# Kernel tuning notes

Hardware: AMD Instinct MI355X
Metric: run time of the kernel (lower is better)

## Reference

```python
import jax, jax.numpy as jnp
import numpy as np

L = 2      # decoder layers
B = 4      # batch
T = 1000   # seq_len (mask built for this length)
C = 768    # input_dim / d_model
H = 12     # num_heads
DK = C // H
WIN = 100


def layernorm(x, g, b):
    m = x.mean(-1, keepdims=True)
    v = x.var(-1, keepdims=True)
    return (x - m) / jnp.sqrt(v + 1e-5) * g + b


def pos_encoding(t, c):
    # Transformer-XL / espnet RelPositionalEncoding table: relative positions t-1 .. -(t-1)
    rel = jnp.arange(t - 1, -t, -1, dtype=jnp.float32)          # (2t-1,)
    div = jnp.exp(-jnp.arange(0, c, 2, dtype=jnp.float32) * (np.log(10000.0) / c))
    ang = rel[:, None] * div[None, :]                            # (2t-1, c/2)
    pe = jnp.zeros((2 * t - 1, c), dtype=jnp.float32)
    pe = pe.at[:, 0::2].set(jnp.sin(ang)).at[:, 1::2].set(jnp.cos(ang))
    return pe


def rel_shift(x):
    # x: (B, H, T, 2T-1) -> (B, H, T, T), Transformer-XL relative shift
    b, h, t, p = x.shape
    xp = jnp.pad(x, ((0, 0), (0, 0), (0, 0), (1, 0)))
    xp = xp.reshape(b, h, p + 1, t)[:, :, 1:, :].reshape(b, h, t, p)
    return xp[..., :t]


def setup_inputs() -> dict:
    key = jax.random.key(0)
    ks = jax.random.split(key, 16)
    s = 0.02
    inp = {
        "x": jax.random.normal(ks[0], (B, T, C), dtype=jnp.float32),
        "Wq": jax.random.normal(ks[1], (L, C, C), dtype=jnp.float32) * s,
        "bq": jnp.zeros((L, C), dtype=jnp.float32),
        "Wk": jax.random.normal(ks[2], (L, C, C), dtype=jnp.float32) * s,
        "bk": jnp.zeros((L, C), dtype=jnp.float32),
        "Wv": jax.random.normal(ks[3], (L, C, C), dtype=jnp.float32) * s,
        "bv": jnp.zeros((L, C), dtype=jnp.float32),
        "Wo": jax.random.normal(ks[4], (L, C, C), dtype=jnp.float32) * s,
        "bo": jnp.zeros((L, C), dtype=jnp.float32),
        "Wp": jax.random.normal(ks[5], (L, C, C), dtype=jnp.float32) * s,   # linear_pos, no bias
        "pos_u": jax.random.normal(ks[6], (L, H, DK), dtype=jnp.float32) * s,
        "pos_v": jax.random.normal(ks[7], (L, H, DK), dtype=jnp.float32) * s,
        "ln1_g": jnp.ones((L, C), dtype=jnp.float32),
        "ln1_b": jnp.zeros((L, C), dtype=jnp.float32),
        "ln2_g": jnp.ones((L, C), dtype=jnp.float32),
        "ln2_b": jnp.zeros((L, C), dtype=jnp.float32),
        "W1": jax.random.normal(ks[8], (L, C, C), dtype=jnp.float32) * s,   # mlp_ratio = 1
        "b1": jnp.zeros((L, C), dtype=jnp.float32),
        "W2": jax.random.normal(ks[9], (L, C, C), dtype=jnp.float32) * s,
        "b2": jnp.zeros((L, C), dtype=jnp.float32),
    }
    # diagonal (banded) mask: True = blocked outside the attention window
    i = np.arange(T)
    blocked = np.abs(i[:, None] - i[None, :]) > (WIN // 2)
    inp["att_mask"] = jnp.asarray(blocked)
    return inp


def reference(x, att_mask, Wq, bq, Wk, bk, Wv, bv, Wo, bo, Wp, pos_u, pos_v,
              ln1_g, ln1_b, ln2_g, ln2_b, W1, b1, W2, b2):
    Bb, t, c = x.shape
    pe = pos_encoding(t, c)                       # (2T-1, C)
    h = x * jnp.sqrt(jnp.float32(c))              # xscale in RelPositionalEncoding
    for l in range(L):
        y = layernorm(h, ln1_g[l], ln1_b[l])
        q = (y @ Wq[l] + bq[l]).reshape(Bb, t, H, DK)
        k = (y @ Wk[l] + bk[l]).reshape(Bb, t, H, DK)
        v = (y @ Wv[l] + bv[l]).reshape(Bb, t, H, DK)
        p = (pe @ Wp[l]).reshape(2 * t - 1, H, DK)
        ac = jnp.einsum('bthd,bshd->bhts', q + pos_u[l], k)
        bd = rel_shift(jnp.einsum('bthd,phd->bhtp', q + pos_v[l], p))
        scores = (ac + bd) / jnp.sqrt(jnp.float32(DK))
        scores = jnp.where(att_mask[None, None], jnp.float32(-1e9), scores)
        attn = jax.nn.softmax(scores, axis=-1)
        o = jnp.einsum('bhts,bshd->bthd', attn, v).reshape(Bb, t, c)
        h = h + (o @ Wo[l] + bo[l])
        y2 = layernorm(h, ln2_g[l], ln2_b[l])
        h = h + (jax.nn.gelu(y2 @ W1[l] + b1[l]) @ W2[l] + b2[l])
    return h
```

## Files before the change

kernel.cpp:

```cpp
#include <hip/hip_runtime.h>
#include <math.h>

#define LNUM 2
#define BBATCH 4
#define TSEQ 1000
#define CDIM 768
#define HHEADS 12
#define DKK 64
#define PPOS (2*TSEQ-1)
#define HALFW 50
#define MROWS (BBATCH*TSEQ)
#define MPAD 4096
#define QKVDIM (3*CDIM)
#define NS 176

typedef __attribute__((ext_vector_type(8))) short s16x8;
typedef __attribute__((ext_vector_type(4))) short s16x4;
typedef __attribute__((ext_vector_type(4))) float f32x4;

#define LDSOFF(p) ((unsigned)(uintptr_t)(__attribute__((address_space(3))) const void*)(p))

__device__ __forceinline__ ushort f2bf(float x) {
    unsigned u = __float_as_uint(x);
    unsigned r = u + 0x7FFFu + ((u >> 16) & 1u);
    return (ushort)(r >> 16);
}
__device__ __forceinline__ float bf2f(ushort h) {
    return __uint_as_float(((unsigned)h) << 16);
}
__device__ __forceinline__ float gelu_f(float x) {
    float u = 0.7978845608028654f * (x + 0.044715f * x * x * x);
    return 0.5f * x * (1.f + tanhf(u));
}
__device__ __forceinline__ void gload_lds16(const void* g, void* l) {
    __builtin_amdgcn_global_load_lds(
        (const __attribute__((address_space(1))) void*)g,
        (__attribute__((address_space(3))) void*)l, 16, 0, 0);
}
__device__ __forceinline__ s16x4 tr_read(unsigned addr) {
    s16x4 d;
    asm volatile("ds_read_b64_tr_b16 %0, %1" : "=v"(d) : "v"(addr));
    return d;
}
__device__ __forceinline__ s16x4 tr_read128(unsigned addr) {
    s16x4 d;
    asm volatile("ds_read_b64_tr_b16 %0, %1 offset:128" : "=v"(d) : "v"(addr));
    return d;
}

__global__ __launch_bounds__(256) void transpose_pack(
    const float* __restrict__ Wq, const float* __restrict__ Wk,
    const float* __restrict__ Wv, const float* __restrict__ Wp,
    const float* __restrict__ Wo, const float* __restrict__ W1,
    const float* __restrict__ W2,
    ushort* __restrict__ Wtqkv, ushort* __restrict__ Wtp,
    ushort* __restrict__ Wto, ushort* __restrict__ Wt1, ushort* __restrict__ Wt2) {
    const int l = blockIdx.z / 7, m = blockIdx.z % 7;
    const float* srcs[7] = {Wq, Wk, Wv, Wp, Wo, W1, W2};
    const float* src = srcs[m] + (size_t)l * CDIM * CDIM;
    ushort* dst;
    if (m < 3)       dst = Wtqkv + (size_t)l * QKVDIM * CDIM + (size_t)m * CDIM * CDIM;
    else if (m == 3) dst = Wtp + (size_t)l * CDIM * CDIM;
    else if (m == 4) dst = Wto + (size_t)l * CDIM * CDIM;
    else if (m == 5) dst = Wt1 + (size_t)l * CDIM * CDIM;
    else             dst = Wt2 + (size_t)l * CDIM * CDIM;
    __shared__ float tile[32][33];
    const int tx = threadIdx.x, ty = threadIdx.y;
    const int c0 = blockIdx.x * 32, r0 = blockIdx.y * 32;
#pragma unroll
    for (int i = 0; i < 4; ++i)
        tile[ty + i * 8][tx] = src[(size_t)(r0 + ty + i * 8) * CDIM + c0 + tx];
    __syncthreads();
#pragma unroll
    for (int i = 0; i < 4; ++i)
        dst[(size_t)(c0 + ty + i * 8) * CDIM + r0 + tx] = f2bf(tile[tx][ty + i * 8]);
}

__global__ __launch_bounds__(256) void prep_small(ushort* __restrict__ pe,
                                                  const float* __restrict__ bq,
                                                  const float* __restrict__ bk,
                                                  const float* __restrict__ bv,
                                                  float* __restrict__ bqkv) {
    int idx = blockIdx.x * 256 + threadIdx.x;
    const int npair = 256 * (CDIM / 2);
    if (idx < npair) {
        int jloc = idx / (CDIM / 2);
        int m = idx - jloc * (CDIM / 2);
        int j = 896 + jloc;
        float rel = (float)(TSEQ - 1 - j);
        float div = expf(-(float)(2 * m) * (9.210340371976184f / (float)CDIM));
        float a = rel * div;
        pe[(size_t)j * CDIM + 2 * m]     = f2bf(sinf(a));
        pe[(size_t)j * CDIM + 2 * m + 1] = f2bf(cosf(a));
    }
    if (idx < LNUM * QKVDIM) {
        int l = idx / QKVDIM, c = idx - l * QKVDIM;
        float v;
        if (c < CDIM)            v = bq[l * CDIM + c];
        else if (c < 2 * CDIM)   v = bk[l * CDIM + c - CDIM];
        else                     v = bv[l * CDIM + c - 2 * CDIM];
        bqkv[idx] = v;
    }
}

__global__ __launch_bounds__(192) void ln_kernel(const float* __restrict__ in,
                                                 const float* __restrict__ g,
                                                 const float* __restrict__ bta,
                                                 ushort* __restrict__ y, float xscale) {
    const int row = blockIdx.x, tid = threadIdx.x;
    float4 v = *(const float4*)&in[(size_t)row * CDIM + tid * 4];
    v.x *= xscale; v.y *= xscale; v.z *= xscale; v.w *= xscale;
    float s  = v.x + v.y + v.z + v.w;
    float ss = v.x * v.x + v.y * v.y + v.z * v.z + v.w * v.w;
#pragma unroll
    for (int off = 32; off; off >>= 1) {
        s  += __shfl_xor(s, off);
        ss += __shfl_xor(ss, off);
    }
    __shared__ float sm[3], sq[3];
    const int wid = tid >> 6, lane = tid & 63;
    if (lane == 0) { sm[wid] = s; sq[wid] = ss; }
    __syncthreads();
    const float st  = sm[0] + sm[1] + sm[2];
    const float sst = sq[0] + sq[1] + sq[2];
    const float mean = st * (1.f / CDIM);
    const float var  = sst * (1.f / CDIM) - mean * mean;
    const float rstd = rsqrtf(var + 1e-5f);
    const float4 g4 = *(const float4*)&g[tid * 4];
    const float4 b4 = *(const float4*)&bta[tid * 4];
    ushort o0 = f2bf((v.x - mean) * rstd * g4.x + b4.x);
    ushort o1 = f2bf((v.y - mean) * rstd * g4.y + b4.y);
    ushort o2 = f2bf((v.z - mean) * rstd * g4.z + b4.z);
    ushort o3 = f2bf((v.w - mean) * rstd * g4.w + b4.w);
    uint2 pk; pk.x = (unsigned)o0 | ((unsigned)o1 << 16);
    pk.y = (unsigned)o2 | ((unsigned)o3 << 16);
    *(uint2*)&y[(size_t)row * CDIM + tid * 4] = pk;
}

template <int EPI>
__global__ __launch_bounds__(256, 3) void gemm64(const ushort* __restrict__ A,
                                                 const ushort* __restrict__ Bt,
                                                 const float* __restrict__ bias,
                                                 void* Out, int M, int ldo,
                                                 const float* resid, float rscale,
                                                 size_t zsB, size_t zsO) {
    __shared__ ushort lds[24576];
    const int tid = threadIdx.x;
    const int w = tid >> 6, lane = tid & 63;
    const int row0 = blockIdx.x * 64, col0 = blockIdx.y * 128;
    const size_t zb = blockIdx.z;
    Bt += zb * zsB;
    if (EPI == 2) Out = (void*)((float*)Out + zb * zsO);
    else          Out = (void*)((ushort*)Out + zb * zsO);

    const int srow8  = lane >> 3;
    const int schunk = (lane & 7) ^ srow8;

#define STAGE64(buf, k0)                                                        \
    {                                                                           \
        _Pragma("unroll")                                                       \
        for (int g = 0; g < 6; ++g) {                                           \
            const int grp = w * 6 + g;                                          \
            const int r = grp * 8 + srow8;                                      \
            const ushort* src = (grp < 8)                                       \
                ? A  + (size_t)(row0 + r) * CDIM + (k0) + schunk * 8            \
                : Bt + (size_t)(col0 + (r - 64)) * CDIM + (k0) + schunk * 8;    \
            gload_lds16(src, (char*)lds + (buf) * 24576 + grp * 1024);          \
        }                                                                       \
    }

    const int wm = (w >> 1) * 32, wn = (w & 1) * 64;
    const int lr = lane & 15, q = lane >> 4;
    f32x4 acc[2][4] = {};

    STAGE64(0, 0);
    __syncthreads();
    int cur = 0;
    for (int k0 = 0; k0 < CDIM; k0 += 64) {
        if (k0 + 64 < CDIM) STAGE64(cur ^ 1, k0 + 64);
        const int base = cur * 12288;
#pragma unroll
        for (int kk = 0; kk < 2; ++kk) {
            s16x8 af[2], bfr[4];
#pragma unroll
            for (int i = 0; i < 2; ++i) {
                const int r = wm + i * 16 + lr;
                af[i] = *(const s16x8*)&lds[base + r * 64 + ((((kk << 2) | q) ^ (r & 7)) << 3)];
            }
#pragma unroll
            for (int j = 0; j < 4; ++j) {
                const int r = 64 + wn + j * 16 + lr;
                bfr[j] = *(const s16x8*)&lds[base + r * 64 + ((((kk << 2) | q) ^ (r & 7)) << 3)];
            }
#pragma unroll
            for (int i = 0; i < 2; ++i)
#pragma unroll
                for (int j = 0; j < 4; ++j)
                    acc[i][j] = __builtin_amdgcn_mfma_f32_16x16x32_bf16(af[i], bfr[j], acc[i][j], 0, 0, 0);
        }
        __syncthreads();
        cur ^= 1;
    }
#undef STAGE64

    const int lrr = (lane >> 4) * 4;
    const int lc = lane & 15;
#pragma unroll
    for (int j = 0; j < 4; ++j) {
        const int col = col0 + wn + j * 16 + lc;
        const float bv = bias ? bias[col] : 0.f;
#pragma unroll
        for (int i = 0; i < 2; ++i) {
#pragma unroll
            for (int r = 0; r < 4; ++r) {
                const int row = row0 + wm + i * 16 + lrr + r;
                if (row >= M) continue;
                const float v = acc[i][j][r] + bv;
                if (EPI == 0)
                    ((ushort*)Out)[(size_t)row * ldo + col] = f2bf(v);
                else if (EPI == 1)
                    ((ushort*)Out)[(size_t)row * ldo + col] = f2bf(gelu_f(v));
                else {
                    float* p = (float*)Out + (size_t)row * ldo + col;
                    *p = resid[(size_t)row * ldo + col] * rscale + v;
                }
            }
        }
    }
}

template <int EPI>
__global__ __launch_bounds__(256, 3) void gemm128(const ushort* __restrict__ A,
                                                  const ushort* __restrict__ Bt,
                                                  const float* __restrict__ bias,
                                                  void* Out, int M, int ldo) {
    __shared__ ushort lds[16384];
    const int tid = threadIdx.x;
    const int w = tid >> 6, lane = tid & 63;
    const int row0 = blockIdx.x * 128, col0 = blockIdx.y * 128;
    const int srow   = lane >> 2;
    const int schunk = (lane & 3) ^ ((lane >> 3) & 3);
    const int wm = (w >> 1) * 64, wn = (w & 1) * 64;
    const int lr = lane & 15, q = lane >> 4;

#define STAGE128(buf, k0)                                                       \
    {                                                                           \
        _Pragma("unroll")                                                       \
        for (int g = 0; g < 4; ++g) {                                           \
            const int sp = w * 4 + g;                                           \
            const int r = sp * 16 + srow;                                       \
            const ushort* src = (r < 128)                                       \
                ? A  + (size_t)(row0 + r) * CDIM + (k0) + schunk * 8            \
                : Bt + (size_t)(col0 + (r - 128)) * CDIM + (k0) + schunk * 8;   \
            gload_lds16(src, (char*)lds + (buf) * 16384 + sp * 1024);           \
        }                                                                       \
    }

    f32x4 acc[4][4] = {};
    STAGE128(0, 0);
    __syncthreads();
    int cur = 0;
    for (int k0 = 0; k0 < CDIM; k0 += 32) {
        if (k0 + 32 < CDIM) STAGE128(cur ^ 1, k0 + 32);
        const int base = cur * 8192;
        s16x8 af[4], bfr[4];
#pragma unroll
        for (int i = 0; i < 4; ++i) {
            const int r = wm + i * 16 + lr;
            af[i] = *(const s16x8*)&lds[base + r * 32 + ((q ^ ((r >> 1) & 3)) << 3)];
        }
#pragma unroll
        for (int j = 0; j < 4; ++j) {
            const int r = 128 + wn + j * 16 + lr;
            bfr[j] = *(const s16x8*)&lds[base + r * 32 + ((q ^ ((r >> 1) & 3)) << 3)];
        }
#pragma unroll
        for (int i = 0; i < 4; ++i)
#pragma unroll
            for (int j = 0; j < 4; ++j)
                acc[i][j] = __builtin_amdgcn_mfma_f32_16x16x32_bf16(af[i], bfr[j], acc[i][j], 0, 0, 0);
        __syncthreads();
        cur ^= 1;
    }
#undef STAGE128

    const int crow0 = row0 + (w >> 1) * 64;
    const int ccol0 = col0 + (w & 1) * 64;
    const int lrr = (lane >> 4) * 4;
    const int lc = lane & 15;
#pragma unroll
    for (int j = 0; j < 4; ++j) {
        const int col = ccol0 + j * 16 + lc;
        const float bv = bias ? bias[col] : 0.f;
#pragma unroll
        for (int i = 0; i < 4; ++i) {
#pragma unroll
            for (int r = 0; r < 4; ++r) {
                const int row = crow0 + i * 16 + lrr + r;
                if (row >= M) continue;
                const float v = acc[i][j][r] + bv;
                if (EPI == 0)
                    ((ushort*)Out)[(size_t)row * ldo + col] = f2bf(v);
                else if (EPI == 1)
                    ((ushort*)Out)[(size_t)row * ldo + col] = f2bf(gelu_f(v));
            }
        }
    }
}

__global__ __launch_bounds__(256, 3) void attn_mfma(
    const ushort* __restrict__ qkv, const ushort* __restrict__ pb,
    const float* __restrict__ pos_u, const float* __restrict__ pos_v,
    ushort* __restrict__ o) {
    __shared__ __align__(16) char smem[51200];
    ushort* Kl   = (ushort*)smem;
    ushort* Pl   = (ushort*)smem;
    ushort* Vsub = (ushort*)(smem + 25600);
    ushort* Bd   = (ushort*)(smem + 37888);

    const int tid = threadIdx.x;
    const int w = tid >> 6, lane = tid & 63;
    const int t0 = blockIdx.x * 64;
    const int h = blockIdx.y, b = blockIdx.z;
    const int m0 = w * 16;
    const int lr = lane & 15, lk = (lane >> 4) * 8, q = lane >> 4;

    auto vsrc = [&](int sp) -> const ushort* {
        const int ob = sp * 1024 + lane * 16;
        const int d0c = ob / 6144;
        const int rem = ob - d0c * 6144;
        const int j = rem >> 5;
        const int halfo = (rem & 31) >> 4;
        int t = t0 - HALFW + j; t = t < 0 ? 0 : (t < TSEQ ? t : TSEQ - 1);
        return qkv + (size_t)(b * TSEQ + t) * QKVDIM + 2 * CDIM + h * DKK
               + (d0c & 1) * 16 + halfo * 8;
    };

    int tq = t0 + m0 + lr; tq = tq < TSEQ ? tq : TSEQ - 1;
    const ushort* qp = qkv + (size_t)(b * TSEQ + tq) * QKVDIM + h * DKK;
    s16x8 qr0 = *(const s16x8*)(qp + lk);
    s16x8 qr1 = *(const s16x8*)(qp + 32 + lk);
    const float* puB = pos_u + h * DKK;
    const float* pvB = pos_v + h * DKK;
    float puA[16], pvA[16];
    *(float4*)&puA[0]  = *(const float4*)(puB + lk);
    *(float4*)&puA[4]  = *(const float4*)(puB + lk + 4);
    *(float4*)&puA[8]  = *(const float4*)(puB + 32 + lk);
    *(float4*)&puA[12] = *(const float4*)(puB + 32 + lk + 4);
    *(float4*)&pvA[0]  = *(const float4*)(pvB + lk);
    *(float4*)&pvA[4]  = *(const float4*)(pvB + lk + 4);
    *(float4*)&pvA[8]  = *(const float4*)(pvB + 32 + lk);
    *(float4*)&pvA[12] = *(const float4*)(pvB + 32 + lk + 4);

    const ushort* pbh = pb + (size_t)949 * CDIM + h * DKK;
    s16x8 pfr[7][2];
#pragma unroll
    for (int uf = 0; uf < 7; ++uf) {
        pfr[uf][0] = *(const s16x8*)&pbh[(size_t)(uf * 16 + lr) * CDIM + lk];
        pfr[uf][1] = *(const s16x8*)&pbh[(size_t)(uf * 16 + lr) * CDIM + 32 + lk];
    }

#pragma unroll
    for (int g = 0; g < 3; ++g) {
        const int sp = w * 3 + g;
        gload_lds16(vsrc(sp), (char*)Vsub + sp * 1024);
    }

    {
        const int srow8 = lane >> 3;
        const int schunk = (lane & 7) ^ srow8;
#pragma unroll
        for (int g = 0; g < 6; ++g) {
            const int sp = w * 6 + g;
            if (sp < 22) {
                const int r = sp * 8 + srow8;
                int kb = t0 - HALFW + r; kb = kb < 0 ? 0 : (kb < TSEQ ? kb : TSEQ - 1);
                const ushort* src = qkv + (size_t)(b * TSEQ + kb) * QKVDIM + CDIM
                                    + h * DKK + schunk * 8;
                gload_lds16(src, (char*)Kl + sp * 1024);
            }
        }
    }

    s16x8 qu0, qu1, qv0, qv1;
#pragma unroll
    for (int e = 0; e < 8; ++e) {
        const float q0 = bf2f((ushort)qr0[e]), q1 = bf2f((ushort)qr1[e]);
        qu0[e] = (short)f2bf(q0 + puA[e]);
        qu1[e] = (short)f2bf(q1 + puA[8 + e]);
        qv0[e] = (short)f2bf(q0 + pvA[e]);
        qv1[e] = (short)f2bf(q1 + pvA[8 + e]);
    }
    __syncthreads();

    const f32x4 zero = {0.f, 0.f, 0.f, 0.f};
    f32x4 acS[11], acB[7];
    __builtin_amdgcn_s_setprio(1);
#pragma unroll
    for (int uf = 0; uf < 7; ++uf) {
        acB[uf] = __builtin_amdgcn_mfma_f32_16x16x32_bf16(qv0, pfr[uf][0], zero, 0, 0, 0);
        acB[uf] = __builtin_amdgcn_mfma_f32_16x16x32_bf16(qv1, pfr[uf][1], acB[uf], 0, 0, 0);
    }
#pragma unroll
    for (int jf = 0; jf < 11; ++jf) {
        const int rr = jf * 16 + lr;
        const int sw = rr & 7;
        s16x8 k0 = *(const s16x8*)&Kl[rr * 64 + (((q)     ^ sw) << 3)];
        s16x8 k1 = *(const s16x8*)&Kl[rr * 64 + (((q | 4) ^ sw) << 3)];
        acS[jf] = __builtin_amdgcn_mfma_f32_16x16x32_bf16(qu0, k0, zero, 0, 0, 0);
        acS[jf] = __builtin_amdgcn_mfma_f32_16x16x32_bf16(qu1, k1, acS[jf], 0, 0, 0);
    }
    __builtin_amdgcn_s_setprio(0);

    ushort* bdw = Bd + w * 16 * 104;
#pragma unroll
    for (int uf = 0; uf < 7; ++uf)
#pragma unroll
        for (int r = 0; r < 4; ++r)
            bdw[((lane >> 4) * 4 + r) * 104 + uf * 16 + lr] = f2bf(acB[uf][r]);
    float mx[4] = {-1e30f, -1e30f, -1e30f, -1e30f};
#pragma unroll
    for (int jf = 0; jf < 11; ++jf)
#pragma unroll
        for (int r = 0; r < 4; ++r) {
            const int tl = (lane >> 4) * 4 + r;
            const int tloc = m0 + tl;
            const int j = jf * 16 + lr;
            const int u = j - tloc;
            const int s = t0 - HALFW + j;
            const bool valid = (u >= 0) & (u <= 2 * HALFW) & (s >= 0) & (s < TSEQ)
                               & (t0 + tloc < TSEQ);
            float sc = -1e30f;
            if (valid) sc = (acS[jf][r] + bf2f(bdw[tl * 104 + u])) * 0.125f;
            acS[jf][r] = sc;
            mx[r] = fmaxf(mx[r], sc);
        }
#pragma unroll
    for (int r = 0; r < 4; ++r)
#pragma unroll
        for (int off = 8; off; off >>= 1)
            mx[r] = fmaxf(mx[r], __shfl_xor(mx[r], off));
    float sm[4] = {0.f, 0.f, 0.f, 0.f};
#pragma unroll
    for (int jf = 0; jf < 11; ++jf)
#pragma unroll
        for (int r = 0; r < 4; ++r) {
            float e = __expf(acS[jf][r] - mx[r]);
            acS[jf][r] = e;
            sm[r] += e;
        }
#pragma unroll
    for (int r = 0; r < 4; ++r) {
#pragma unroll
        for (int off = 8; off; off >>= 1) sm[r] += __shfl_xor(sm[r], off);
        sm[r] = 1.f / sm[r];
    }
    __syncthreads();

    s16x8 vr0 = *vsrc(12 + w * 3 + 0);
    s16x8 vr1 = *vsrc(12 + w * 3 + 1);
    s16x8 vr2 = *vsrc(12 + w * 3 + 2);

#pragma unroll
    for (int jf = 0; jf < 11; ++jf)
#pragma unroll
        for (int r = 0; r < 4; ++r)
            Pl[(m0 + (lane >> 4) * 4 + r) * 200 + jf * 16 + lr] = f2bf(acS[jf][r]);
#pragma unroll
    for (int r = 0; r < 4; ++r)
        Pl[(m0 + (lane >> 4) * 4 + r) * 200 + 176 + lr] = 0;

    s16x8 pa[6];
#pragma unroll
    for (int ks = 0; ks < 6; ++ks)
        pa[ks] = *(const s16x8*)&Pl[(m0 + lr) * 200 + ks * 32 + lk];

    const unsigned vbase = LDSOFF(Vsub);
#pragma unroll
    for (int nf = 0; nf < 2; ++nf) {
        const unsigned abase = vbase + (nf & 1) * 6144 + ((lane >> 4) << 8) + ((lane & 15) << 1);
        s16x4 lo[6], hi[6];
#pragma unroll
        for (int ks = 0; ks < 6; ++ks) {
            lo[ks] = tr_read(abase + ks * 1024);
            hi[ks] = tr_read128(abase + ks * 1024);
        }
        asm volatile("s_waitcnt lgkmcnt(0)" ::: "memory");
        __builtin_amdgcn_sched_barrier(0);
        f32x4 acO = {};
        __builtin_amdgcn_s_setprio(1);
#pragma unroll
        for (int ks = 0; ks < 6; ++ks) {
            s16x8 vb = __builtin_shufflevector(lo[ks], hi[ks], 0, 1, 2, 3, 4, 5, 6, 7);
            acO = __builtin_amdgcn_mfma_f32_16x16x32_bf16(pa[ks], vb, acO, 0, 0, 0);
        }
        __builtin_amdgcn_s_setprio(0);
#pragma unroll
        for (int r = 0; r < 4; ++r) {
            const int t = t0 + m0 + (lane >> 4) * 4 + r;
            if (t < TSEQ)
                o[(size_t)(b * TSEQ + t) * CDIM + h * DKK + nf * 16 + lr] =
                    f2bf(acO[r] * sm[r]);
        }
    }
    __syncthreads();

    *(s16x8*)((char*)Vsub + (w * 3 + 0) * 1024 + lane * 16) = vr0;
    *(s16x8*)((char*)Vsub + (w * 3 + 1) * 1024 + lane * 16) = vr1;
    *(s16x8*)((char*)Vsub + (w * 3 + 2) * 1024 + lane * 16) = vr2;
    __syncthreads();

#pragma unroll
    for (int nf = 2; nf < 4; ++nf) {
        const unsigned abase = vbase + (nf & 1) * 6144 + ((lane >> 4) << 8) + ((lane & 15) << 1);
        s16x4 lo[6], hi[6];
#pragma unroll
        for (int ks = 0; ks < 6; ++ks) {
            lo[ks] = tr_read(abase + ks * 1024);
            hi[ks] = tr_read128(abase + ks * 1024);
        }
        asm volatile("s_waitcnt lgkmcnt(0)" ::: "memory");
        __builtin_amdgcn_sched_barrier(0);
        f32x4 acO = {};
        __builtin_amdgcn_s_setprio(1);
#pragma unroll
        for (int ks = 0; ks < 6; ++ks) {
            s16x8 vb = __builtin_shufflevector(lo[ks], hi[ks], 0, 1, 2, 3, 4, 5, 6, 7);
            acO = __builtin_amdgcn_mfma_f32_16x16x32_bf16(pa[ks], vb, acO, 0, 0, 0);
        }
        __builtin_amdgcn_s_setprio(0);
#pragma unroll
        for (int r = 0; r < 4; ++r) {
            const int t = t0 + m0 + (lane >> 4) * 4 + r;
            if (t < TSEQ)
                o[(size_t)(b * TSEQ + t) * CDIM + h * DKK + nf * 16 + lr] =
                    f2bf(acO[r] * sm[r]);
        }
    }
}

extern "C" void kernel_launch(void* const* d_in, const int* in_sizes, int n_in,
                              void* d_out, int out_size, void* d_ws, size_t ws_size,
                              hipStream_t stream) {
    const float* x     = (const float*)d_in[0];
    const float* Wq    = (const float*)d_in[1];
    const float* bq    = (const float*)d_in[2];
    const float* Wk    = (const float*)d_in[3];
    const float* bk    = (const float*)d_in[4];
    const float* Wv    = (const float*)d_in[5];
    const float* bv    = (const float*)d_in[6];
    const float* Wo    = (const float*)d_in[7];
    const float* bo    = (const float*)d_in[8];
    const float* Wp    = (const float*)d_in[9];
    const float* pos_u = (const float*)d_in[10];
    const float* pos_v = (const float*)d_in[11];
    const float* ln1g  = (const float*)d_in[12];
    const float* ln1b  = (const float*)d_in[13];
    const float* ln2g  = (const float*)d_in[14];
    const float* ln2b  = (const float*)d_in[15];
    const float* W1    = (const float*)d_in[16];
    const float* b1    = (const float*)d_in[17];
    const float* W2    = (const float*)d_in[18];
    const float* b2    = (const float*)d_in[19];

    float* h = (float*)d_out;
    const float XS = 27.712812921102035f;

    char* p = (char*)d_ws;
    ushort* Wtqkv = (ushort*)p;               p += (size_t)LNUM * QKVDIM * CDIM * 2;
    ushort* Wtp   = (ushort*)p;               p += (size_t)LNUM * CDIM * CDIM * 2;
    ushort* Wto   = (ushort*)p;               p += (size_t)LNUM * CDIM * CDIM * 2;
    ushort* Wt1   = (ushort*)p;               p += (size_t)LNUM * CDIM * CDIM * 2;
    ushort* Wt2   = (ushort*)p;               p += (size_t)LNUM * CDIM * CDIM * 2;
    float*  bqkv  = (float*)p;                p += (size_t)LNUM * QKVDIM * 4;
    ushort* pe    = (ushort*)p;               p += (size_t)2048 * CDIM * 2;
    ushort* pb    = (ushort*)p;               p += (size_t)LNUM * 2048 * CDIM * 2;
    ushort* y     = (ushort*)p;               p += (size_t)MPAD * CDIM * 2;
    ushort* qkv   = (ushort*)p;               p += (size_t)MPAD * QKVDIM * 2;
    ushort* o     = (ushort*)p;               p += (size_t)MPAD * CDIM * 2;
    ushort* hid   = (ushort*)p;               p += (size_t)MPAD * CDIM * 2;

    transpose_pack<<<dim3(24, 24, LNUM * 7), dim3(32, 8), 0, stream>>>(
        Wq, Wk, Wv, Wp, Wo, W1, W2, Wtqkv, Wtp, Wto, Wt1, Wt2);
    prep_small<<<384, 256, 0, stream>>>(pe, bq, bk, bv, bqkv);

    const int MB = (MROWS + 63) / 64;
    const dim3 gQKV(32, QKVDIM / 128);
    const dim3 gC(MB, CDIM / 128);
    const dim3 gP(4, CDIM / 128, LNUM);
    const dim3 gA(16, HHEADS, BBATCH);

    gemm64<0><<<gP, 256, 0, stream>>>(pe + (size_t)896 * CDIM, Wtp, nullptr,
                                      pb + (size_t)896 * CDIM, 256, CDIM,
                                      nullptr, 0.f,
                                      (size_t)CDIM * CDIM, (size_t)2048 * CDIM);

    for (int l = 0; l < LNUM; ++l) {
        const size_t wo = (size_t)l * CDIM * CDIM;
        const float* res1 = (l == 0) ? x : h;
        const float rs1   = (l == 0) ? XS : 1.f;
        ln_kernel<<<MROWS, 192, 0, stream>>>(res1, ln1g + l * CDIM, ln1b + l * CDIM, y, rs1);
        gemm128<0><<<gQKV, 256, 0, stream>>>(y, Wtqkv + (size_t)l * QKVDIM * CDIM,
                                             bqkv + l * QKVDIM, qkv, MROWS, QKVDIM);
        attn_mfma<<<gA, 256, 0, stream>>>(
            qkv, pb + (size_t)l * 2048 * CDIM,
            pos_u + l * HHEADS * DKK, pos_v + l * HHEADS * DKK, o);
        gemm64<2><<<gC, 256, 0, stream>>>(o, Wto + wo, bo + l * CDIM, h, MROWS, CDIM,
                                          res1, rs1, 0, 0);
        ln_kernel<<<MROWS, 192, 0, stream>>>(h, ln2g + l * CDIM, ln2b + l * CDIM, y, 1.f);
        gemm64<1><<<gC, 256, 0, stream>>>(y, Wt1 + wo, b1 + l * CDIM, hid, MROWS, CDIM,
                                          nullptr, 0.f, 0, 0);
        gemm64<2><<<gC, 256, 0, stream>>>(hid, Wt2 + wo, b2 + l * CDIM, h, MROWS, CDIM,
                                          h, 1.f, 0, 0);
    }
}
```

Baseline: 257.3 us.

## Fuse prep kernels, vectorize weight transpose, add XCD-aware tile swizzle in GEMMs

Merges the small positional-encoding/bias prep kernel into the weight transpose kernel as an extra z-slice, saving one launch. The transpose now uses float4 loads and packed bf16 stores. The GEMM kernels remap workgroup IDs so neighbouring output tiles are placed on the same XCD, aiming for better L2 reuse. The attention kernel moves its positional fragment loads after the K/V staging, to shorten register live ranges or overlap loads.

```diff
diff --git a/kernel.cpp b/kernel.cpp
--- a/kernel.cpp
+++ b/kernel.cpp
@@ -47,6 +47,11 @@
     asm volatile("ds_read_b64_tr_b16 %0, %1 offset:128" : "=v"(d) : "v"(addr));
     return d;
 }
+__device__ __forceinline__ int xcd_swz(int orig, int nwg) {
+    const int xcd = orig & 7, ixc = orig >> 3;
+    const int qq = nwg >> 3, rr = nwg & 7;
+    return (xcd < rr ? xcd * (qq + 1) : rr * (qq + 1) + (xcd - rr) * qq) + ixc;
+}
 
 __global__ __launch_bounds__(256) void transpose_pack(
     const float* __restrict__ Wq, const float* __restrict__ Wk,
@@ -54,7 +59,35 @@
     const float* __restrict__ Wo, const float* __restrict__ W1,
     const float* __restrict__ W2,
     ushort* __restrict__ Wtqkv, ushort* __restrict__ Wtp,
-    ushort* __restrict__ Wto, ushort* __restrict__ Wt1, ushort* __restrict__ Wt2) {
+    ushort* __restrict__ Wto, ushort* __restrict__ Wt1, ushort* __restrict__ Wt2,
+    ushort* __restrict__ pe,
+    const float* __restrict__ bq, const float* __restrict__ bk,
+    const float* __restrict__ bv, float* __restrict__ bqkv) {
+    const int tx = threadIdx.x, ty = threadIdx.y;
+    if (blockIdx.z == 14) {
+        const int linear = blockIdx.y * 24 + blockIdx.x;
+        const int idx = linear * 256 + ty * 8 + tx;
+        const int npair = 256 * (CDIM / 2);
+        if (idx < npair) {
+            int jloc = idx / (CDIM / 2);
+            int m = idx - jloc * (CDIM / 2);
+            int j = 896 + jloc;
+            float rel = (float)(TSEQ - 1 - j);
+            float div = expf(-(float)(2 * m) * (9.210340371976184f / (float)CDIM));
+            float a = rel * div;
+            pe[(size_t)j * CDIM + 2 * m]     = f2bf(sinf(a));
+            pe[(size_t)j * CDIM + 2 * m + 1] = f2bf(cosf(a));
+        }
+        if (idx < LNUM * QKVDIM) {
+            int l = idx / QKVDIM, c = idx - l * QKVDIM;
+            float v;
+            if (c < CDIM)            v = bq[l * CDIM + c];
+            else if (c < 2 * CDIM)   v = bk[l * CDIM + c - CDIM];
+            else                     v = bv[l * CDIM + c - 2 * CDIM];
+            bqkv[idx] = v;
+        }
+        return;
+    }
     const int l = blockIdx.z / 7, m = blockIdx.z % 7;
     const float* srcs[7] = {Wq, Wk, Wv, Wp, Wo, W1, W2};
     const float* src = srcs[m] + (size_t)l * CDIM * CDIM;
@@ -65,42 +98,19 @@
     else if (m == 5) dst = Wt1 + (size_t)l * CDIM * CDIM;
     else             dst = Wt2 + (size_t)l * CDIM * CDIM;
     __shared__ float tile[32][33];
-    const int tx = threadIdx.x, ty = threadIdx.y;
     const int c0 = blockIdx.x * 32, r0 = blockIdx.y * 32;
-#pragma unroll
-    for (int i = 0; i < 4; ++i)
-        tile[ty + i * 8][tx] = src[(size_t)(r0 + ty + i * 8) * CDIM + c0 + tx];
-    __syncthreads();
-#pragma unroll
-    for (int i = 0; i < 4; ++i)
-        dst[(size_t)(c0 + ty + i * 8) * CDIM + r0 + tx] = f2bf(tile[tx][ty + i * 8]);
-}
-
-__global__ __launch_bounds__(256) void prep_small(ushort* __restrict__ pe,
-                                                  const float* __restrict__ bq,
-                                                  const float* __restrict__ bk,
-                                                  const float* __restrict__ bv,
-                                                  float* __restrict__ bqkv) {
-    int idx = blockIdx.x * 256 + threadIdx.x;
-    const int npair = 256 * (CDIM / 2);
-    if (idx < npair) {
-        int jloc = idx / (CDIM / 2);
-        int m = idx - jloc * (CDIM / 2);
-        int j = 896 + jloc;
-        float rel = (float)(TSEQ - 1 - j);
-        float div = expf(-(float)(2 * m) * (9.210340371976184f / (float)CDIM));
-        float a = rel * div;
-        pe[(size_t)j * CDIM + 2 * m]     = f2bf(sinf(a));
-        pe[(size_t)j * CDIM + 2 * m + 1] = f2bf(cosf(a));
-    }
-    if (idx < LNUM * QKVDIM) {
-        int l = idx / QKVDIM, c = idx - l * QKVDIM;
-        float v;
-        if (c < CDIM)            v = bq[l * CDIM + c];
-        else if (c < 2 * CDIM)   v = bk[l * CDIM + c - CDIM];
-        else                     v = bv[l * CDIM + c - 2 * CDIM];
-        bqkv[idx] = v;
-    }
+    const float4 v = *(const float4*)&src[(size_t)(r0 + ty) * CDIM + c0 + tx * 4];
+    tile[tx * 4 + 0][ty] = v.x;
+    tile[tx * 4 + 1][ty] = v.y;
+    tile[tx * 4 + 2][ty] = v.z;
+    tile[tx * 4 + 3][ty] = v.w;
+    __syncthreads();
+    const float a0 = tile[ty][tx * 4 + 0], a1 = tile[ty][tx * 4 + 1];
+    const float a2 = tile[ty][tx * 4 + 2], a3 = tile[ty][tx * 4 + 3];
+    uint2 pk;
+    pk.x = (unsigned)f2bf(a0) | ((unsigned)f2bf(a1) << 16);
+    pk.y = (unsigned)f2bf(a2) | ((unsigned)f2bf(a3) << 16);
+    *(uint2*)&dst[(size_t)(c0 + ty) * CDIM + r0 + tx * 4] = pk;
 }
 
 __global__ __launch_bounds__(192) void ln_kernel(const float* __restrict__ in,
@@ -147,7 +157,10 @@
     __shared__ ushort lds[24576];
     const int tid = threadIdx.x;
     const int w = tid >> 6, lane = tid & 63;
-    const int row0 = blockIdx.x * 64, col0 = blockIdx.y * 128;
+    const int nwg = gridDim.x * gridDim.y;
+    const int newid = xcd_swz(blockIdx.y * gridDim.x + blockIdx.x, nwg);
+    const int col0 = (newid % gridDim.y) * 128;
+    const int row0 = (newid / gridDim.y) * 64;
     const size_t zb = blockIdx.z;
     Bt += zb * zsB;
     if (EPI == 2) Out = (void*)((float*)Out + zb * zsO);
@@ -237,7 +250,10 @@
     __shared__ ushort lds[16384];
     const int tid = threadIdx.x;
     const int w = tid >> 6, lane = tid & 63;
-    const int row0 = blockIdx.x * 128, col0 = blockIdx.y * 128;
+    const int nwg = gridDim.x * gridDim.y;
+    const int newid = xcd_swz(blockIdx.y * gridDim.x + blockIdx.x, nwg);
+    const int col0 = (newid % gridDim.y) * 128;
+    const int row0 = (newid / gridDim.y) * 128;
     const int srow   = lane >> 2;
     const int schunk = (lane & 3) ^ ((lane >> 3) & 3);
     const int wm = (w >> 1) * 64, wn = (w & 1) * 64;
@@ -352,20 +368,11 @@
     *(float4*)&pvA[8]  = *(const float4*)(pvB + 32 + lk);
     *(float4*)&pvA[12] = *(const float4*)(pvB + 32 + lk + 4);
 
-    const ushort* pbh = pb + (size_t)949 * CDIM + h * DKK;
-    s16x8 pfr[7][2];
-#pragma unroll
-    for (int uf = 0; uf < 7; ++uf) {
-        pfr[uf][0] = *(const s16x8*)&pbh[(size_t)(uf * 16 + lr) * CDIM + lk];
-        pfr[uf][1] = *(const s16x8*)&pbh[(size_t)(uf * 16 + lr) * CDIM + 32 + lk];
-    }
-
 #pragma unroll
     for (int g = 0; g < 3; ++g) {
         const int sp = w * 3 + g;
         gload_lds16(vsrc(sp), (char*)Vsub + sp * 1024);
     }
-
     {
         const int srow8 = lane >> 3;
         const int schunk = (lane & 7) ^ srow8;
@@ -390,6 +397,14 @@
         qu1[e] = (short)f2bf(q1 + puA[8 + e]);
         qv0[e] = (short)f2bf(q0 + pvA[e]);
         qv1[e] = (short)f2bf(q1 + pvA[8 + e]);
+    }
+
+    const ushort* pbh = pb + (size_t)949 * CDIM + h * DKK;
+    s16x8 pfr[7][2];
+#pragma unroll
+    for (int uf = 0; uf < 7; ++uf) {
+        pfr[uf][0] = *(const s16x8*)&pbh[(size_t)(uf * 16 + lr) * CDIM + lk];
+        pfr[uf][1] = *(const s16x8*)&pbh[(size_t)(uf * 16 + lr) * CDIM + 32 + lk];
     }
     __syncthreads();
 
@@ -580,9 +595,9 @@
     ushort* o     = (ushort*)p;               p += (size_t)MPAD * CDIM * 2;
     ushort* hid   = (ushort*)p;               p += (size_t)MPAD * CDIM * 2;
 
-    transpose_pack<<<dim3(24, 24, LNUM * 7), dim3(32, 8), 0, stream>>>(
-        Wq, Wk, Wv, Wp, Wo, W1, W2, Wtqkv, Wtp, Wto, Wt1, Wt2);
-    prep_small<<<384, 256, 0, stream>>>(pe, bq, bk, bv, bqkv);
+    transpose_pack<<<dim3(24, 24, 15), dim3(8, 32), 0, stream>>>(
+        Wq, Wk, Wv, Wp, Wo, W1, W2, Wtqkv, Wtp, Wto, Wt1, Wt2,
+        pe, bq, bk, bv, bqkv);
 
     const int MB = (MROWS + 63) / 64;
     const dim3 gQKV(32, QKVDIM / 128);
```

Measured after the change: 246.9 us, median of 2. 1.04x faster.
